# Kernel tuning notes

Measured on AMD Instinct MI355X. Metric: run time of the kernel, lower is better.

## Reference

```python
import jax, jax.numpy as jnp
import numpy as np

B, T = 1, 600            # batch_size, seq_len (ms)
U = 10                   # n_bkg_units
N_V1, N_LM = 200000, 50000
NNZ_V1, NNZ_LM = 800000, 200000   # neurons * n_bkg_connections(=4)
LAM = 1000.0 / 1000.0    # bkg_units_firing_rate / 1000 -> Poisson rate per ms


def setup_inputs() -> dict:
    key = jax.random.key(0)
    ks = jax.random.split(key, 7)
    inp = jax.random.normal(ks[0], (B, T, 1), dtype=jnp.float32)
    w_v1 = jax.random.normal(ks[1], (NNZ_V1,), dtype=jnp.float32)
    rows_v1 = jax.random.randint(ks[2], (NNZ_V1,), 0, N_V1, dtype=jnp.int32)
    cols_v1 = jax.random.randint(ks[3], (NNZ_V1,), 0, U, dtype=jnp.int32)
    w_lm = jax.random.normal(ks[4], (NNZ_LM,), dtype=jnp.float32)
    rows_lm = jax.random.randint(ks[5], (NNZ_LM,), 0, N_LM, dtype=jnp.int32)
    cols_lm = jax.random.randint(ks[6], (NNZ_LM,), 0, U, dtype=jnp.int32)
    return {"inp": inp, "w_v1": w_v1, "rows_v1": rows_v1, "cols_v1": cols_v1,
            "w_lm": w_lm, "rows_lm": rows_lm, "cols_lm": cols_lm}


def _column_current(spikes, w, rows, cols, n_neurons):
    # Scatter COO weights into a dense (n_neurons, U) matrix (duplicates sum,
    # matching tf.sparse semantics); U is tiny so this is cheap, then a single
    # GEMM reproduces sparse_dense_matmul(W, spikes^T)^T exactly.
    W = jnp.zeros((n_neurons, U), dtype=spikes.dtype).at[rows, cols].add(w)
    i_in = spikes @ W.T                      # (B*T, n_neurons)
    return i_in.reshape(B, T, n_neurons)


def reference(inp, w_v1, rows_v1, cols_v1, w_lm, rows_lm, cols_lm):
    # Poisson background spikes, fixed key for determinism. inp only sets seq_len.
    pkey = jax.random.key(42)
    spikes = jax.random.poisson(pkey, LAM, (B * T, U)).astype(jnp.float32)
    v1 = _column_current(spikes, w_v1, rows_v1, cols_v1, N_V1)   # (B,T,N_V1)
    lm = _column_current(spikes, w_lm, rows_lm, cols_lm, N_LM)   # (B,T,N_LM)
    return jnp.concatenate([v1, lm], axis=-1)                    # (B,T,N_V1+N_LM)
```

## Files before the change

kernel.cpp:

```cpp
#include <hip/hip_runtime.h>
#include <stdint.h>

#define NV1 200000
#define NLM 50000
#define NTOT 250000
#define TLEN 600
#define UU 10
#define NNZV1 800000
#define NNZLM 200000
#define NNZTOT (NNZV1 + NNZLM)
#define NELEM (TLEN * UU)

#define BINSHIFT 9
#define BINROWS 512
#define NB 489
#define CAP 2560
#define BBLK 256
#define BPT 16

#define SLOTS_OFF   0ULL
#define SPIKES2_OFF 10014720ULL
#define BINCNT_OFF  10038720ULL
#define WS_NEED_SORT 10040676ULL
#define WT_OFF      0ULL
#define SPIKES_OFF  10000000ULL
#define WS_NEED_FALLBACK 10024000ULL

typedef float f32x4 __attribute__((ext_vector_type(4)));
typedef float f32x2 __attribute__((ext_vector_type(2)));
typedef unsigned long long u64;

__device__ __forceinline__ void tf2x32(uint32_t k0, uint32_t k1,
                                       uint32_t c0, uint32_t c1,
                                       uint32_t& o0, uint32_t& o1) {
  const uint32_t ks2 = k0 ^ k1 ^ 0x1BD11BDAu;
  uint32_t x0 = c0 + k0;
  uint32_t x1 = c1 + k1;
#define TF_RND(r) { x0 += x1; x1 = (x1 << (r)) | (x1 >> (32 - (r))); x1 ^= x0; }
  TF_RND(13) TF_RND(15) TF_RND(26) TF_RND(6)
  x0 += k1;  x1 += ks2 + 1u;
  TF_RND(17) TF_RND(29) TF_RND(16) TF_RND(24)
  x0 += ks2; x1 += k0 + 2u;
  TF_RND(13) TF_RND(15) TF_RND(26) TF_RND(6)
  x0 += k0;  x1 += k1 + 3u;
  TF_RND(17) TF_RND(29) TF_RND(16) TF_RND(24)
  x0 += k1;  x1 += ks2 + 4u;
  TF_RND(13) TF_RND(15) TF_RND(26) TF_RND(6)
  x0 += ks2; x1 += k0 + 5u;
#undef TF_RND
  o0 = x0; o1 = x1;
}

__device__ __forceinline__ int spike_value(int e) {
  uint32_t r0 = 0u, r1 = 42u;
  float S = 0.0f;
  int result = 63;
  for (int iter = 0; iter < 64; ++iter) {
    uint32_t n0, n1, s0, s1;
    tf2x32(r0, r1, 0u, 0u, n0, n1);
    tf2x32(r0, r1, 0u, 1u, s0, s1);
    r0 = n0; r1 = n1;
    uint32_t h0, h1;
    tf2x32(s0, s1, 0u, (uint32_t)e, h0, h1);
    const uint32_t bits = h0 ^ h1;
    const float u = __uint_as_float((bits >> 9) | 0x3f800000u) - 1.0f;
    S += logf(u);
    if (!(S > -1.0f)) { result = iter; break; }
  }
  return result;
}

__device__ __forceinline__ void load_nnz(int i,
                                         const float* __restrict__ wv, const int* __restrict__ rv,
                                         const int* __restrict__ cv,
                                         const float* __restrict__ wl, const int* __restrict__ rl,
                                         const int* __restrict__ cl,
                                         int& grow, int& col, float& w) {
  if (i < NNZV1) { grow = rv[i]; col = cv[i]; w = wv[i]; }
  else { const int j = i - NNZV1; grow = NV1 + rl[j]; col = cl[j]; w = wl[j]; }
}

#define SB ((NELEM + 255) / 256)
__global__ void __launch_bounds__(256) k1_spikes(float* __restrict__ spikes,
                                                 uint32_t* __restrict__ binCount) {
  const int gid = blockIdx.x * 256 + threadIdx.x;
  if (gid < NB) binCount[gid] = 0u;
  if (gid < NELEM) spikes[gid] = (float)spike_value(gid);
}

__global__ void __launch_bounds__(256) k3_bin(const float* __restrict__ wv, const int* __restrict__ rv,
                                              const int* __restrict__ cv,
                                              const float* __restrict__ wl, const int* __restrict__ rl,
                                              const int* __restrict__ cl,
                                              uint32_t* __restrict__ binCount,
                                              u64* __restrict__ slots) {
  __shared__ uint32_t hist[512];
  __shared__ uint32_t cur[512];
  const int t = threadIdx.x;
  hist[t] = 0u; hist[t + 256] = 0u;
  __syncthreads();
  const int base = blockIdx.x * (256 * BPT);
  u64 pk[BPT];
#pragma unroll
  for (int r = 0; r < BPT; ++r) {
    const int i = base + r * 256 + t;
    pk[r] = ~0ULL;
    if (i < NNZTOT) {
      int grow, col; float w;
      load_nnz(i, wv, rv, cv, wl, rl, cl, grow, col, w);
      pk[r] = ((u64)((uint32_t)grow | ((uint32_t)col << 18)) << 32) |
              (u64)__float_as_uint(w);
      atomicAdd(&hist[grow >> BINSHIFT], 1u);
    }
  }
  __syncthreads();
  for (int b = t; b < NB; b += 256) {
    const uint32_t h = hist[b];
    cur[b] = h ? atomicAdd(&binCount[b], h) : 0u;
  }
  __syncthreads();
#pragma unroll
  for (int r = 0; r < BPT; ++r) {
    if (pk[r] != ~0ULL) {
      const uint32_t rc = (uint32_t)(pk[r] >> 32);
      const int bin = (int)((rc & 0x3FFFFu) >> BINSHIFT);
      const uint32_t pos = atomicAdd(&cur[bin], 1u);
      if (pos < CAP) slots[(size_t)bin * CAP + pos] = pk[r];
    }
  }
}

#define SROW 12
__global__ void __launch_bounds__(256) k5_fused(const u64* __restrict__ slots,
                                                const uint32_t* __restrict__ binCount,
                                                const float* __restrict__ spikes,
                                                float* __restrict__ out) {
  __shared__ float acc[BINROWS * UU];
  __shared__ float s[TLEN * SROW];
  const int t = threadIdx.x;
  const int bin = blockIdx.x;
  const int row0 = bin << BINSHIFT;

  for (int i = t; i < BINROWS * UU; i += 256) acc[i] = 0.f;
  for (int i = t; i < TLEN * SROW; i += 256) {
    const int row = i / SROW, u = i - row * SROW;
    s[i] = (u < UU) ? spikes[row * UU + u] : 0.f;
  }
  __syncthreads();

  int cnt = (int)binCount[bin];
  if (cnt > CAP) cnt = CAP;
  const u64* sl = slots + (size_t)bin * CAP;
  for (int i = t; i < cnt; i += 256) {
    const u64 v = sl[i];
    const uint32_t rc = (uint32_t)(v >> 32);
    const float w = __uint_as_float((uint32_t)v);
    atomicAdd(&acc[((int)(rc & 0x3FFFFu) - row0) * UU + (int)(rc >> 18)], w);
  }
  __syncthreads();

  const int n = row0 + t * 2;
  if (n >= NTOT) return;
  float w[2][UU];
#pragma unroll
  for (int r = 0; r < 2; ++r)
#pragma unroll
    for (int u = 0; u < UU; ++u)
      w[r][u] = acc[(t * 2 + r) * UU + u];

  float* op = out + n;
  for (int tt = 0; tt < TLEN; ++tt) {
    const f32x4 sA = *reinterpret_cast<const f32x4*>(&s[tt * SROW]);
    const f32x4 sB = *reinterpret_cast<const f32x4*>(&s[tt * SROW + 4]);
    const f32x2 sC = *reinterpret_cast<const f32x2*>(&s[tt * SROW + 8]);
    f32x2 a;
#pragma unroll
    for (int r = 0; r < 2; ++r) {
      float x = sA.x * w[r][0];
      x = fmaf(sA.y, w[r][1], x);
      x = fmaf(sA.z, w[r][2], x);
      x = fmaf(sA.w, w[r][3], x);
      x = fmaf(sB.x, w[r][4], x);
      x = fmaf(sB.y, w[r][5], x);
      x = fmaf(sB.z, w[r][6], x);
      x = fmaf(sB.w, w[r][7], x);
      x = fmaf(sC.x, w[r][8], x);
      x = fmaf(sC.y, w[r][9], x);
      a[r] = x;
    }
    __builtin_nontemporal_store(a, reinterpret_cast<f32x2*>(op));
    op += NTOT;
  }
}

#define WZ4 (NTOT * UU / 4)
#define ZB  ((WZ4 + 255) / 256)
__global__ void __launch_bounds__(256) init_kernel(f32x4* __restrict__ W4,
                                                   float* __restrict__ spikes) {
  const int b = blockIdx.x;
  if (b < ZB) {
    const int i = b * 256 + threadIdx.x;
    if (i < WZ4) W4[i] = (f32x4)(0.f);
    return;
  }
  const int e = (b - ZB) * 256 + threadIdx.x;
  if (e >= NELEM) return;
  spikes[e] = (float)spike_value(e);
}

__global__ void scatter_kernel(const float* __restrict__ w_v1,
                               const int* __restrict__ rows_v1,
                               const int* __restrict__ cols_v1,
                               const float* __restrict__ w_lm,
                               const int* __restrict__ rows_lm,
                               const int* __restrict__ cols_lm,
                               float* __restrict__ WT) {
  const int i = blockIdx.x * blockDim.x + threadIdx.x;
  if (i >= NNZTOT) return;
  if (i < NNZV1) {
    atomicAdd(&WT[(size_t)cols_v1[i] * NTOT + rows_v1[i]], w_v1[i]);
  } else {
    const int j = i - NNZV1;
    atomicAdd(&WT[(size_t)cols_lm[j] * NTOT + NV1 + rows_lm[j]], w_lm[j]);
  }
}

#define TTILE 75
#define NT4 (NTOT / 4)
__global__ void __launch_bounds__(256, 8) out_kernel(const float* __restrict__ WT,
                                                     const float* __restrict__ spikes,
                                                     float* __restrict__ out) {
  __shared__ float s[TTILE * SROW];
  const int t0 = blockIdx.y * TTILE;
  for (int i = threadIdx.x; i < TTILE * SROW; i += 256) {
    const int row = i / SROW, u = i - row * SROW;
    s[i] = (u < UU) ? spikes[(t0 + row) * UU + u] : 0.f;
  }
  __syncthreads();

  const int n4 = blockIdx.x * 256 + threadIdx.x;
  if (n4 >= NT4) return;
  const int n = n4 * 4;

  f32x4 w[UU];
#pragma unroll
  for (int u = 0; u < UU; ++u)
    w[u] = *reinterpret_cast<const f32x4*>(&WT[(size_t)u * NTOT + n]);

  float* op = &out[(size_t)t0 * NTOT + n];
  for (int t = 0; t < TTILE; ++t) {
    const f32x4 sA = *reinterpret_cast<const f32x4*>(&s[t * SROW]);
    const f32x4 sB = *reinterpret_cast<const f32x4*>(&s[t * SROW + 4]);
    const f32x2 sC = *reinterpret_cast<const f32x2*>(&s[t * SROW + 8]);
    f32x4 acc = sA.x * w[0];
    acc += sA.y * w[1];
    acc += sA.z * w[2];
    acc += sA.w * w[3];
    acc += sB.x * w[4];
    acc += sB.y * w[5];
    acc += sB.z * w[6];
    acc += sB.w * w[7];
    acc += sC.x * w[8];
    acc += sC.y * w[9];
    __builtin_nontemporal_store(acc, reinterpret_cast<f32x4*>(op));
    op += NTOT;
  }
}

extern "C" void kernel_launch(void* const* d_in, const int* in_sizes, int n_in,
                              void* d_out, int out_size, void* d_ws, size_t ws_size,
                              hipStream_t stream) {
  const float* w_v1    = (const float*)d_in[1];
  const int*   rows_v1 = (const int*)d_in[2];
  const int*   cols_v1 = (const int*)d_in[3];
  const float* w_lm    = (const float*)d_in[4];
  const int*   rows_lm = (const int*)d_in[5];
  const int*   cols_lm = (const int*)d_in[6];
  float* out = (float*)d_out;

  char* ws = (char*)d_ws;

  if (ws_size >= WS_NEED_SORT) {
    u64*      slots    = (u64*)(ws + SLOTS_OFF);
    float*    spikes   = (float*)(ws + SPIKES2_OFF);
    uint32_t* binCount = (uint32_t*)(ws + BINCNT_OFF);
    k1_spikes<<<SB, 256, 0, stream>>>(spikes, binCount);
    k3_bin<<<BBLK, 256, 0, stream>>>(w_v1, rows_v1, cols_v1,
                                     w_lm, rows_lm, cols_lm, binCount, slots);
    k5_fused<<<NB, 256, 0, stream>>>(slots, binCount, spikes, out);
  } else if (ws_size >= WS_NEED_FALLBACK) {
    float* WT     = (float*)(ws + WT_OFF);
    float* spikes = (float*)(ws + SPIKES_OFF);
    init_kernel<<<ZB + SB, 256, 0, stream>>>((f32x4*)WT, spikes);
    scatter_kernel<<<(NNZTOT + 255) / 256, 256, 0, stream>>>(w_v1, rows_v1, cols_v1,
                                                             w_lm, rows_lm, cols_lm, WT);
    dim3 grid((NT4 + 255) / 256, TLEN / TTILE);
    out_kernel<<<grid, 256, 0, stream>>>(WT, spikes, out);
  }
}
```

Before: 168.2 us.

## Widen bins to 1024 rows, split time across two blocks, store 16B vectors

Doubles the rows per bin so each thread in the fused kernel computes four neurons and writes 16-byte non-temporal stores instead of 8-byte ones. The time axis is split into two halves handled by separate blocks, which keeps the grid size roughly the same and halves the spike tile in shared memory. Spikes are now written pre-padded to a 12-wide layout so the shared-memory fill is a straight vector copy. Each split block redoes the slot accumulation for its bin, and the larger accumulator raises LDS use, which may lower occupancy.

```diff
diff --git a/kernel.cpp b/kernel.cpp
--- a/kernel.cpp
+++ b/kernel.cpp
@@ -11,17 +11,20 @@
 #define NNZTOT (NNZV1 + NNZLM)
 #define NELEM (TLEN * UU)
 
-#define BINSHIFT 9
-#define BINROWS 512
-#define NB 489
-#define CAP 2560
-#define BBLK 256
-#define BPT 16
+#define BINSHIFT 10
+#define BINROWS 1024
+#define NB 245
+#define CAP 4608
+#define BBLK 512
+#define BPT 8
+
+#define TSPLIT 2
+#define THALF (TLEN / TSPLIT)
 
 #define SLOTS_OFF   0ULL
-#define SPIKES2_OFF 10014720ULL
-#define BINCNT_OFF  10038720ULL
-#define WS_NEED_SORT 10040676ULL
+#define SPIKES2_OFF 9031680ULL
+#define BINCNT_OFF  9060480ULL
+#define WS_NEED_SORT 9061460ULL
 #define WT_OFF      0ULL
 #define SPIKES_OFF  10000000ULL
 #define WS_NEED_FALLBACK 10024000ULL
@@ -80,12 +83,15 @@
   else { const int j = i - NNZV1; grow = NV1 + rl[j]; col = cl[j]; w = wl[j]; }
 }
 
-#define SB ((NELEM + 255) / 256)
-__global__ void __launch_bounds__(256) k1_spikes(float* __restrict__ spikes,
+#define SB ((TLEN * 12 + 255) / 256)
+__global__ void __launch_bounds__(256) k1_spikes(float* __restrict__ spikes_p,
                                                  uint32_t* __restrict__ binCount) {
   const int gid = blockIdx.x * 256 + threadIdx.x;
   if (gid < NB) binCount[gid] = 0u;
-  if (gid < NELEM) spikes[gid] = (float)spike_value(gid);
+  if (gid < TLEN * 12) {
+    const int row = gid / 12, u = gid - row * 12;
+    spikes_p[gid] = (u < UU) ? (float)spike_value(row * UU + u) : 0.f;
+  }
 }
 
 __global__ void __launch_bounds__(256) k3_bin(const float* __restrict__ wv, const int* __restrict__ rv,
@@ -94,10 +100,10 @@
                                               const int* __restrict__ cl,
                                               uint32_t* __restrict__ binCount,
                                               u64* __restrict__ slots) {
-  __shared__ uint32_t hist[512];
-  __shared__ uint32_t cur[512];
+  __shared__ uint32_t hist[256];
+  __shared__ uint32_t cur[256];
   const int t = threadIdx.x;
-  hist[t] = 0u; hist[t + 256] = 0u;
+  hist[t] = 0u;
   __syncthreads();
   const int base = blockIdx.x * (256 * BPT);
   u64 pk[BPT];
@@ -114,9 +120,9 @@
     }
   }
   __syncthreads();
-  for (int b = t; b < NB; b += 256) {
-    const uint32_t h = hist[b];
-    cur[b] = h ? atomicAdd(&binCount[b], h) : 0u;
+  if (t < NB) {
+    const uint32_t h = hist[t];
+    cur[t] = h ? atomicAdd(&binCount[t], h) : 0u;
   }
   __syncthreads();
 #pragma unroll
@@ -133,18 +139,21 @@
 #define SROW 12
 __global__ void __launch_bounds__(256) k5_fused(const u64* __restrict__ slots,
                                                 const uint32_t* __restrict__ binCount,
-                                                const float* __restrict__ spikes,
+                                                const float* __restrict__ spikes_p,
                                                 float* __restrict__ out) {
   __shared__ float acc[BINROWS * UU];
-  __shared__ float s[TLEN * SROW];
+  __shared__ float s[THALF * SROW];
   const int t = threadIdx.x;
-  const int bin = blockIdx.x;
+  const int bin  = blockIdx.x >> 1;
+  const int half = blockIdx.x & 1;
   const int row0 = bin << BINSHIFT;
+  const int tt0  = half * THALF;
 
   for (int i = t; i < BINROWS * UU; i += 256) acc[i] = 0.f;
-  for (int i = t; i < TLEN * SROW; i += 256) {
-    const int row = i / SROW, u = i - row * SROW;
-    s[i] = (u < UU) ? spikes[row * UU + u] : 0.f;
+  {
+    const f32x4* src = reinterpret_cast<const f32x4*>(spikes_p + tt0 * SROW);
+    f32x4* dst = reinterpret_cast<f32x4*>(s);
+    for (int i = t; i < THALF * SROW / 4; i += 256) dst[i] = src[i];
   }
   __syncthreads();
 
@@ -159,23 +168,23 @@
   }
   __syncthreads();
 
-  const int n = row0 + t * 2;
+  const int n = row0 + t * 4;
   if (n >= NTOT) return;
-  float w[2][UU];
-#pragma unroll
-  for (int r = 0; r < 2; ++r)
+  float w[4][UU];
+#pragma unroll
+  for (int r = 0; r < 4; ++r)
 #pragma unroll
     for (int u = 0; u < UU; ++u)
-      w[r][u] = acc[(t * 2 + r) * UU + u];
-
-  float* op = out + n;
-  for (int tt = 0; tt < TLEN; ++tt) {
-    const f32x4 sA = *reinterpret_cast<const f32x4*>(&s[tt * SROW]);
-    const f32x4 sB = *reinterpret_cast<const f32x4*>(&s[tt * SROW + 4]);
-    const f32x2 sC = *reinterpret_cast<const f32x2*>(&s[tt * SROW + 8]);
-    f32x2 a;
-#pragma unroll
-    for (int r = 0; r < 2; ++r) {
+      w[r][u] = acc[(t * 4 + r) * UU + u];
+
+  float* op = out + (size_t)tt0 * NTOT + n;
+  for (int tl = 0; tl < THALF; ++tl) {
+    const f32x4 sA = *reinterpret_cast<const f32x4*>(&s[tl * SROW]);
+    const f32x4 sB = *reinterpret_cast<const f32x4*>(&s[tl * SROW + 4]);
+    const f32x2 sC = *reinterpret_cast<const f32x2*>(&s[tl * SROW + 8]);
+    f32x4 a;
+#pragma unroll
+    for (int r = 0; r < 4; ++r) {
       float x = sA.x * w[r][0];
       x = fmaf(sA.y, w[r][1], x);
       x = fmaf(sA.z, w[r][2], x);
@@ -188,13 +197,14 @@
       x = fmaf(sC.y, w[r][9], x);
       a[r] = x;
     }
-    __builtin_nontemporal_store(a, reinterpret_cast<f32x2*>(op));
+    __builtin_nontemporal_store(a, reinterpret_cast<f32x4*>(op));
     op += NTOT;
   }
 }
 
 #define WZ4 (NTOT * UU / 4)
 #define ZB  ((WZ4 + 255) / 256)
+#define SBF ((NELEM + 255) / 256)
 __global__ void __launch_bounds__(256) init_kernel(f32x4* __restrict__ W4,
                                                    float* __restrict__ spikes) {
   const int b = blockIdx.x;
@@ -282,16 +292,16 @@
 
   if (ws_size >= WS_NEED_SORT) {
     u64*      slots    = (u64*)(ws + SLOTS_OFF);
-    float*    spikes   = (float*)(ws + SPIKES2_OFF);
+    float*    spikes_p = (float*)(ws + SPIKES2_OFF);
     uint32_t* binCount = (uint32_t*)(ws + BINCNT_OFF);
-    k1_spikes<<<SB, 256, 0, stream>>>(spikes, binCount);
+    k1_spikes<<<SB, 256, 0, stream>>>(spikes_p, binCount);
     k3_bin<<<BBLK, 256, 0, stream>>>(w_v1, rows_v1, cols_v1,
                                      w_lm, rows_lm, cols_lm, binCount, slots);
-    k5_fused<<<NB, 256, 0, stream>>>(slots, binCount, spikes, out);
+    k5_fused<<<NB * TSPLIT, 256, 0, stream>>>(slots, binCount, spikes_p, out);
   } else if (ws_size >= WS_NEED_FALLBACK) {
     float* WT     = (float*)(ws + WT_OFF);
     float* spikes = (float*)(ws + SPIKES_OFF);
-    init_kernel<<<ZB + SB, 256, 0, stream>>>((f32x4*)WT, spikes);
+    init_kernel<<<ZB + SBF, 256, 0, stream>>>((f32x4*)WT, spikes);
     scatter_kernel<<<(NNZTOT + 255) / 256, 256, 0, stream>>>(w_v1, rows_v1, cols_v1,
                                                              w_lm, rows_lm, cols_lm, WT);
     dim3 grid((NT4 + 255) / 256, TLEN / TTILE);
```

After: 153.9 us. 1.09x faster.
